# Performance work log

Hardware: AMD Instinct MI355X
Metric: run time of the kernel (lower is better)

The kernel has to match this reference:

```python
import jax, jax.numpy as jnp
import numpy as np

N, E, IN, H, L, NB, G = 50000, 300000, 64, 256, 4, 181, 64
EPS = 1e-5
NEG_SLOPE = 0.2


def segment_softmax(e, seg, n):
    m = jax.ops.segment_max(e, seg, num_segments=n)
    a = jnp.exp(e - m[seg])
    d = jax.ops.segment_sum(a, seg, num_segments=n)
    return a / d[seg]


def setup_inputs() -> dict:
    key = jax.random.key(0)
    ks = jax.random.split(key, 32)
    p = lambda k, shape, fan: (jax.random.normal(k, shape, jnp.float32) / np.sqrt(fan)).astype(jnp.float32)
    inp = {}
    inp["x"] = jax.random.normal(ks[0], (N, IN), jnp.float32)
    inp["edge_index"] = jax.random.randint(ks[1], (2, E), 0, N, jnp.int64)
    inp["batch"] = jnp.sort(jax.random.randint(ks[2], (N,), 0, G, jnp.int64))
    inp["W_in"] = p(ks[3], (H, IN), IN); inp["b_in"] = jnp.zeros((H,), jnp.float32)
    inp["Wl"] = p(ks[4], (L, H, H), H); inp["bl"] = jnp.zeros((L, H), jnp.float32)
    inp["Wr"] = p(ks[5], (L, H, H), H); inp["br"] = jnp.zeros((L, H), jnp.float32)
    inp["att"] = p(ks[6], (L, H), H)
    inp["bias_c"] = jnp.zeros((L, H), jnp.float32)
    inp["ln_g"] = jnp.ones((L, H), jnp.float32); inp["ln_b"] = jnp.zeros((L, H), jnp.float32)
    inp["Wg1"] = p(ks[7], (H, H), H); inp["bg1"] = jnp.zeros((H,), jnp.float32)
    inp["Wg2"] = p(ks[8], (1, H), H); inp["bg2"] = jnp.zeros((1,), jnp.float32)
    inp["Ws"] = p(ks[9], (H, H), H); inp["bs"] = jnp.zeros((H,), jnp.float32)
    inp["Wc"] = p(ks[10], (NB, H), H); inp["bc"] = jnp.zeros((NB,), jnp.float32)
    inp["Wr1"] = p(ks[11], (128, H), H); inp["br1"] = jnp.zeros((128,), jnp.float32)
    inp["Wr2"] = p(ks[12], (1, 128), 128); inp["br2"] = jnp.zeros((1,), jnp.float32)
    return inp


def reference(x, edge_index, batch, W_in, b_in, Wl, bl, Wr, br, att, bias_c, ln_g, ln_b,
              Wg1, bg1, Wg2, bg2, Ws, bs, Wc, bc, Wr1, br1, Wr2, br2):
    n = x.shape[0]
    x = x @ W_in.T + b_in  # input projection -> [N,H]
    loops = jnp.arange(n)
    src = jnp.concatenate([edge_index[0], loops])  # GATv2 add_self_loops=True
    dst = jnp.concatenate([edge_index[1], loops])
    for l in range(L):
        x_res = x
        xl = x @ Wl[l].T + bl[l]  # lin_l (source)
        xr = x @ Wr[l].T + br[l]  # lin_r (target)
        h = jax.nn.leaky_relu(xl[src] + xr[dst], NEG_SLOPE)  # [E+N, H]
        e = h @ att[l]                                       # [E+N]
        alpha = segment_softmax(e, dst, n)
        out = jax.ops.segment_sum(alpha[:, None] * xl[src], dst, num_segments=n) + bias_c[l]
        mu = out.mean(-1, keepdims=True)
        var = out.var(-1, keepdims=True)
        out = (out - mu) / jnp.sqrt(var + EPS) * ln_g[l] + ln_b[l]
        x = jax.nn.relu(out) + x_res  # dropout is identity at eval
    gate = jax.nn.relu(x @ Wg1.T + bg1) @ Wg2.T + bg2  # [N,1]
    a = segment_softmax(gate[:, 0], batch, G)
    pooled = jax.ops.segment_sum(a[:, None] * x, batch, num_segments=G)  # [G,H]
    z = jax.nn.relu(pooled @ Ws.T + bs)
    cls_logits = z @ Wc.T + bc                                   # [G,NB]
    residual = jnp.tanh(jax.nn.relu(z @ Wr1.T + br1) @ Wr2.T + br2)[:, 0]  # [G]
    return cls_logits, residual
```

## Files before the change

### kernel.cpp

```cpp
#include <hip/hip_runtime.h>
#include <math.h>

#define N_NODES 50000
#define N_EDGES 300000
#define IN_DIM 64
#define H 256
#define LAYERS 4
#define NB 181
#define NGRAPH 64
#define EE (N_EDGES + N_NODES)
#define NEG_SLOPE 0.2f
#define LN_EPS 1e-5f

typedef unsigned short u16;
typedef __attribute__((ext_vector_type(8))) _Float16 half8;
typedef __attribute__((ext_vector_type(4))) float floatx4;
typedef __attribute__((ext_vector_type(2))) _Float16 h2;

__device__ __forceinline__ u16 f2h(float f) {
  _Float16 h = (_Float16)f;
  return __builtin_bit_cast(u16, h);
}
__device__ __forceinline__ float h2f(u16 b) {
  return (float)__builtin_bit_cast(_Float16, b);
}
__device__ __forceinline__ h2 u2h2(unsigned int u) {
  return __builtin_bit_cast(h2, u);
}
__device__ __forceinline__ float fdot2f(h2 a, h2 b, float c) {
  typedef __attribute__((ext_vector_type(2))) __fp16 hb;
  return __builtin_amdgcn_fdot2(__builtin_bit_cast(hb, a),
                                __builtin_bit_cast(hb, b), c, false);
}

__device__ __forceinline__ float wave_reduce_sum(float v) {
  #pragma unroll
  for (int off = 32; off > 0; off >>= 1) v += __shfl_xor(v, off, 64);
  return v;
}

__device__ __forceinline__ float half_reduce_sum(float v) {
  v += __shfl_xor(v, 1, 64);
  v += __shfl_xor(v, 2, 64);
  v += __shfl_xor(v, 4, 64);
  v += __shfl_xor(v, 8, 64);
  v += __shfl_xor(v, 16, 64);
  return v;
}

__global__ void cast_weights_kernel(
    const float* __restrict__ Wg1,
    const float* __restrict__ Wl, const float* __restrict__ Wr,
    u16* __restrict__ wg1_h, u16* __restrict__ wl_h, u16* __restrict__ wr_h)
{
  int i = blockIdx.x * 256 + threadIdx.x;
  int which = blockIdx.y;
  const float* s; u16* dd; int n4;
  if (which == 0)      { s = Wg1;  dd = wg1_h; n4 = H * H / 4; }
  else if (which == 1) { s = Wl;   dd = wl_h;  n4 = LAYERS * H * H / 4; }
  else                 { s = Wr;   dd = wr_h;  n4 = LAYERS * H * H / 4; }
  if (i < n4) {
    float4 f = ((const float4*)s)[i];
    ushort4 o;
    o.x = f2h(f.x); o.y = f2h(f.y); o.z = f2h(f.z); o.w = f2h(f.w);
    ((ushort4*)dd)[i] = o;
  }
}

__global__ void init_kernel(int* __restrict__ cnt,
                            float* __restrict__ gate, const float* __restrict__ bg2,
                            const int* __restrict__ batch,
                            int* __restrict__ gstart, int* __restrict__ gend) {
  int i = blockIdx.x * 256 + threadIdx.x;
  if (i < N_NODES) {
    cnt[i] = 1;
    gate[i] = bg2[0];
    int b = batch[i];
    if (i == 0 || batch[i - 1] != b) gstart[b] = i;
    if (i == N_NODES - 1 || batch[i + 1] != b) gend[b] = i + 1;
  }
}

__global__ void count_edges_kernel(const int* __restrict__ dst, int* __restrict__ cnt) {
  int e = blockIdx.x * 256 + threadIdx.x;
  if (e < N_EDGES) atomicAdd(&cnt[dst[e]], 1);
}

__global__ void scan_blocks_kernel(const int* __restrict__ cnt, int* __restrict__ partial,
                                   int* __restrict__ bsums, int n) {
  __shared__ int buf[256];
  int tid = threadIdx.x;
  int i = blockIdx.x * 256 + tid;
  buf[tid] = (i < n) ? cnt[i] : 0;
  __syncthreads();
  #pragma unroll
  for (int off = 1; off < 256; off <<= 1) {
    int t = (tid >= off) ? buf[tid - off] : 0;
    __syncthreads();
    buf[tid] += t;
    __syncthreads();
  }
  if (i < n) partial[i] = buf[tid];
  if (tid == 255) bsums[blockIdx.x] = buf[255];
}

__global__ void scan_sums_kernel(int* __restrict__ bsums, int nblk) {
  __shared__ int buf[256];
  int tid = threadIdx.x;
  buf[tid] = (tid < nblk) ? bsums[tid] : 0;
  __syncthreads();
  #pragma unroll
  for (int off = 1; off < 256; off <<= 1) {
    int t = (tid >= off) ? buf[tid - off] : 0;
    __syncthreads();
    buf[tid] += t;
    __syncthreads();
  }
  if (tid < nblk) bsums[tid] = buf[tid];
}

__global__ void scan_write_kernel(const int* __restrict__ partial, const int* __restrict__ bsums,
                                  const int* __restrict__ cnt,
                                  int* __restrict__ rowp, int* __restrict__ col,
                                  int* __restrict__ fillpos, int n) {
  int i = blockIdx.x * 256 + threadIdx.x;
  if (i < n) {
    int b = blockIdx.x;
    int off = (b > 0) ? bsums[b - 1] : 0;
    int r1 = partial[i] + off;
    rowp[i + 1] = r1;
    if (i == 0) rowp[0] = 0;
    int p = r1 - cnt[i];
    col[p] = i;
    fillpos[i] = p + 1;
  }
}

__global__ void fill_edges_kernel(const int* __restrict__ src, const int* __restrict__ dst,
                                  int* __restrict__ fillpos, int* __restrict__ col) {
  int e = blockIdx.x * 256 + threadIdx.x;
  if (e < N_EDGES) {
    int d = dst[e];
    int p = atomicAdd(&fillpos[d], 1);
    col[p] = src[e];
  }
}

#define GTM 128
#define GTK 64
#define LDB 72
#define SSTR 132

__global__ __launch_bounds__(256) void gemm_proj_kernel(
    const float* __restrict__ A, const float* __restrict__ W,
    const float* __restrict__ bias, u16* __restrict__ outh, int M)
{
  __shared__ u16 smem[2 * GTM * LDB];
  u16* As = smem;
  u16* Bs = smem + GTM * LDB;
  int tid = threadIdx.x;
  int lane = tid & 63;
  int wave = tid >> 6;
  int wm = (wave >> 1) * 64;
  int wn = (wave & 1) * 64;
  int bm = blockIdx.y * GTM;
  int n0 = blockIdx.x * 128;

  floatx4 zero4 = {0.f, 0.f, 0.f, 0.f};
  floatx4 acc[4][4];
  #pragma unroll
  for (int i = 0; i < 4; i++)
    #pragma unroll
    for (int j = 0; j < 4; j++) acc[i][j] = zero4;

  int q8 = (lane >> 4) * 8;
  int mrow = lane & 15;

  {
    int r0 = tid >> 4;
    int c4 = (tid & 15) * 4;
    #pragma unroll
    for (int p = 0; p < 8; p++) {
      int row = r0 + p * 16;
      int gr = bm + row;
      float4 av = {0.f, 0.f, 0.f, 0.f};
      if (gr < M) av = *(const float4*)&A[(size_t)gr * IN_DIM + c4];
      ushort4 oa;
      oa.x = f2h(av.x); oa.y = f2h(av.y); oa.z = f2h(av.z); oa.w = f2h(av.w);
      *(ushort4*)&As[row * LDB + c4] = oa;
      float4 bv = *(const float4*)&W[(size_t)(n0 + row) * IN_DIM + c4];
      ushort4 ob;
      ob.x = f2h(bv.x); ob.y = f2h(bv.y); ob.z = f2h(bv.z); ob.w = f2h(bv.w);
      *(ushort4*)&Bs[row * LDB + c4] = ob;
    }
  }
  __syncthreads();
  #pragma unroll
  for (int h = 0; h < 2; h++) {
    half8 af[4], bf[4];
    #pragma unroll
    for (int i = 0; i < 4; i++)
      af[i] = *(const half8*)&As[(wm + i * 16 + mrow) * LDB + h * 32 + q8];
    #pragma unroll
    for (int j = 0; j < 4; j++)
      bf[j] = *(const half8*)&Bs[(wn + j * 16 + mrow) * LDB + h * 32 + q8];
    #pragma unroll
    for (int i = 0; i < 4; i++)
      #pragma unroll
      for (int j = 0; j < 4; j++)
        acc[i][j] = __builtin_amdgcn_mfma_f32_16x16x32_f16(af[i], bf[j], acc[i][j], 0, 0, 0);
  }

  __syncthreads();
  u16* stage = smem;
  int ccol = lane & 15;
  int crow4 = (lane >> 4) * 4;
  #pragma unroll
  for (int j = 0; j < 4; j++) {
    float bv = bias[n0 + wn + j * 16 + ccol];
    #pragma unroll
    for (int i = 0; i < 4; i++) {
      #pragma unroll
      for (int r = 0; r < 4; r++) {
        int row = wm + i * 16 + crow4 + r;
        stage[row * SSTR + wn + j * 16 + ccol] = f2h(acc[i][j][r] + bv);
      }
    }
  }
  __syncthreads();
  int rr = tid >> 1;
  int c0 = (tid & 1) * 64;
  int grow = bm + rr;
  if (grow < M) {
    const ushort4* sp = (const ushort4*)&stage[rr * SSTR + c0];
    ushort4* gp = (ushort4*)&outh[(size_t)grow * H + n0 + c0];
    #pragma unroll
    for (int q = 0; q < 16; q++) gp[q] = sp[q];
  }
}

#define DTM 64
#define SSTR2 132

__global__ __launch_bounds__(256) void gemm_dual3_kernel(
    const u16* __restrict__ A, const u16* __restrict__ Wlb, const u16* __restrict__ Wrb,
    const float* __restrict__ biasL, const float* __restrict__ biasR,
    u16* __restrict__ outL, u16* __restrict__ outR, int M)
{
  __shared__ u16 As[DTM * LDB];
  __shared__ u16 Bs[128 * LDB];
  int tid = threadIdx.x;
  int lane = tid & 63;
  int wave = tid >> 6;
  int wn = wave * 32;
  int nt = blockIdx.x;
  int bm = blockIdx.y * DTM;
  const u16* W = (nt < 2) ? Wlb : Wrb;
  const float* bias = (nt < 2) ? biasL : biasR;
  u16* outp = (nt < 2) ? outL : outR;
  int n0 = (nt & 1) * 128;
  int mrow = lane & 15;
  int q8 = (lane >> 4) * 8;
  int ccol = lane & 15;
  int crow4 = (lane >> 4) * 4;
  int lr = tid >> 3;
  int lc = (tid & 7) * 8;

  floatx4 zero4 = {0.f, 0.f, 0.f, 0.f};
  floatx4 acc[4][2];
  #pragma unroll
  for (int i = 0; i < 4; i++) {
    acc[i][0] = zero4;
    acc[i][1] = zero4;
  }

  for (int k0 = 0; k0 < H; k0 += 64) {
    __syncthreads();
    #pragma unroll
    for (int p = 0; p < 2; p++) {
      int row = lr + p * 32;
      int gr = bm + row;
      uint4 av = {0, 0, 0, 0};
      if (gr < M) av = *(const uint4*)&A[(size_t)gr * H + k0 + lc];
      *(uint4*)&As[row * LDB + lc] = av;
    }
    #pragma unroll
    for (int p = 0; p < 4; p++) {
      int row = lr + p * 32;
      uint4 bv = *(const uint4*)&W[(size_t)(n0 + row) * H + k0 + lc];
      *(uint4*)&Bs[row * LDB + lc] = bv;
    }
    __syncthreads();
    #pragma unroll
    for (int h = 0; h < 2; h++) {
      half8 af[4], bf[2];
      #pragma unroll
      for (int i = 0; i < 4; i++)
        af[i] = *(const half8*)&As[(i * 16 + mrow) * LDB + h * 32 + q8];
      #pragma unroll
      for (int j = 0; j < 2; j++)
        bf[j] = *(const half8*)&Bs[(wn + j * 16 + mrow) * LDB + h * 32 + q8];
      #pragma unroll
      for (int i = 0; i < 4; i++)
        #pragma unroll
        for (int j = 0; j < 2; j++)
          acc[i][j] = __builtin_amdgcn_mfma_f32_16x16x32_f16(af[i], bf[j], acc[i][j], 0, 0, 0);
    }
  }

  __syncthreads();
  u16* stage = Bs;
  #pragma unroll
  for (int j = 0; j < 2; j++) {
    float bv = bias[n0 + wn + j * 16 + ccol];
    #pragma unroll
    for (int i = 0; i < 4; i++) {
      #pragma unroll
      for (int r = 0; r < 4; r++) {
        int row = i * 16 + crow4 + r;
        stage[row * SSTR2 + wn + j * 16 + ccol] = f2h(acc[i][j][r] + bv);
      }
    }
  }
  __syncthreads();
  #pragma unroll
  for (int pass = 0; pass < 4; pass++) {
    int row = pass * 16 + (tid >> 4);
    int cu = (tid & 15) * 8;
    int grow = bm + row;
    if (grow < M) {
      *(uint4*)&outp[(size_t)grow * H + n0 + cu] =
          *(const uint4*)&stage[row * SSTR2 + cu];
    }
  }
}

__global__ __launch_bounds__(256) void gemm_gate2_kernel(
    const u16* __restrict__ A, const u16* __restrict__ W,
    const float* __restrict__ bias, const float* __restrict__ Wg2,
    float* __restrict__ gate, int M)
{
  __shared__ u16 As[DTM * LDB];
  __shared__ u16 Bs[128 * LDB];
  int tid = threadIdx.x;
  int lane = tid & 63;
  int wave = tid >> 6;
  int wn = wave * 32;
  int n0 = blockIdx.x * 128;
  int bm = blockIdx.y * DTM;
  int mrow = lane & 15;
  int q8 = (lane >> 4) * 8;
  int ccol = lane & 15;
  int crow4 = (lane >> 4) * 4;
  int lr = tid >> 3;
  int lc = (tid & 7) * 8;

  floatx4 zero4 = {0.f, 0.f, 0.f, 0.f};
  floatx4 acc[4][2];
  #pragma unroll
  for (int i = 0; i < 4; i++) {
    acc[i][0] = zero4;
    acc[i][1] = zero4;
  }

  for (int k0 = 0; k0 < H; k0 += 64) {
    __syncthreads();
    #pragma unroll
    for (int p = 0; p < 2; p++) {
      int row = lr + p * 32;
      int gr = bm + row;
      uint4 av = {0, 0, 0, 0};
      if (gr < M) av = *(const uint4*)&A[(size_t)gr * H + k0 + lc];
      *(uint4*)&As[row * LDB + lc] = av;
    }
    #pragma unroll
    for (int p = 0; p < 4; p++) {
      int row = lr + p * 32;
      uint4 bv = *(const uint4*)&W[(size_t)(n0 + row) * H + k0 + lc];
      *(uint4*)&Bs[row * LDB + lc] = bv;
    }
    __syncthreads();
    #pragma unroll
    for (int h = 0; h < 2; h++) {
      half8 af[4], bf[2];
      #pragma unroll
      for (int i = 0; i < 4; i++)
        af[i] = *(const half8*)&As[(i * 16 + mrow) * LDB + h * 32 + q8];
      #pragma unroll
      for (int j = 0; j < 2; j++)
        bf[j] = *(const half8*)&Bs[(wn + j * 16 + mrow) * LDB + h * 32 + q8];
      #pragma unroll
      for (int i = 0; i < 4; i++)
        #pragma unroll
        for (int j = 0; j < 2; j++)
          acc[i][j] = __builtin_amdgcn_mfma_f32_16x16x32_f16(af[i], bf[j], acc[i][j], 0, 0, 0);
    }
  }

  float bv[2], wv[2];
  #pragma unroll
  for (int j = 0; j < 2; j++) {
    int c = n0 + wn + j * 16 + ccol;
    bv[j] = bias[c];
    wv[j] = Wg2[c];
  }
  #pragma unroll
  for (int i = 0; i < 4; i++) {
    #pragma unroll
    for (int r = 0; r < 4; r++) {
      float p = fmaxf(acc[i][0][r] + bv[0], 0.f) * wv[0]
              + fmaxf(acc[i][1][r] + bv[1], 0.f) * wv[1];
      p += __shfl_xor(p, 1, 64);
      p += __shfl_xor(p, 2, 64);
      p += __shfl_xor(p, 4, 64);
      p += __shfl_xor(p, 8, 64);
      int row = bm + i * 16 + crow4 + r;
      if ((lane & 15) == 0 && row < M) atomicAdd(&gate[row], p);
    }
  }
}

__global__ __launch_bounds__(256) void layer_fused_kernel(
    const u16* __restrict__ xl, const u16* __restrict__ xr,
    u16* __restrict__ xst,
    const int* __restrict__ rowp, const int* __restrict__ col,
    const float* __restrict__ att, const float* __restrict__ bias_c,
    const float* __restrict__ ln_g, const float* __restrict__ ln_b)
{
  int lane = threadIdx.x & 63;
  int v = blockIdx.x * 4 + (threadIdx.x >> 6);
  if (v >= N_NODES) return;
  int half = lane >> 5;
  int f8 = (lane & 31) << 3;

  float4 attA = *(const float4*)&att[f8];
  float4 attB = *(const float4*)&att[f8 + 4];
  h2 att0, att1, att2, att3;
  att0[0] = (_Float16)attA.x; att0[1] = (_Float16)attA.y;
  att1[0] = (_Float16)attA.z; att1[1] = (_Float16)attA.w;
  att2[0] = (_Float16)attB.x; att2[1] = (_Float16)attB.y;
  att3[0] = (_Float16)attB.z; att3[1] = (_Float16)attB.w;
  h2 nsl; nsl[0] = (_Float16)NEG_SLOPE; nsl[1] = (_Float16)NEG_SLOPE;

  size_t rowbase = (size_t)v * H + f8;
  uint4 xru = *(const uint4*)&xr[rowbase];
  h2 xr0 = u2h2(xru.x), xr1 = u2h2(xru.y), xr2 = u2h2(xru.z), xr3 = u2h2(xru.w);
  int beg = rowp[v], end = rowp[v + 1];

  uint4 su = *(const uint4*)&xl[rowbase];
  h2 s0 = u2h2(su.x), s1 = u2h2(su.y), s2 = u2h2(su.z), s3 = u2h2(su.w);
  float m;
  {
    h2 t; float pe = 0.f;
    t = s0 + xr0; t = __builtin_elementwise_max(t, t * nsl); pe = fdot2f(t, att0, pe);
    t = s1 + xr1; t = __builtin_elementwise_max(t, t * nsl); pe = fdot2f(t, att1, pe);
    t = s2 + xr2; t = __builtin_elementwise_max(t, t * nsl); pe = fdot2f(t, att2, pe);
    t = s3 + xr3; t = __builtin_elementwise_max(t, t * nsl); pe = fdot2f(t, att3, pe);
    m = half_reduce_sum(pe);
  }
  float wself = half ? 0.f : 1.f;
  float d = wself;
  float o0 = wself * (float)s0[0], o1 = wself * (float)s0[1];
  float o2 = wself * (float)s1[0], o3 = wself * (float)s1[1];
  float o4 = wself * (float)s2[0], o5 = wself * (float)s2[1];
  float o6 = wself * (float)s3[0], o7 = wself * (float)s3[1];

  int p = beg + 1;
  for (; p + 4 <= end; p += 4) {
    int ua = col[p + half];
    int ub = col[p + 2 + half];
    uint4 A = *(const uint4*)&xl[(size_t)ua * H + f8];
    uint4 B = *(const uint4*)&xl[(size_t)ub * H + f8];
    h2 a0 = u2h2(A.x), a1 = u2h2(A.y), a2 = u2h2(A.z), a3 = u2h2(A.w);
    h2 b0 = u2h2(B.x), b1 = u2h2(B.y), b2 = u2h2(B.z), b3 = u2h2(B.w);
    float pa = 0.f, pb = 0.f;
    {
      h2 t;
      t = a0 + xr0; t = __builtin_elementwise_max(t, t * nsl); pa = fdot2f(t, att0, pa);
      t = b0 + xr0; t = __builtin_elementwise_max(t, t * nsl); pb = fdot2f(t, att0, pb);
      t = a1 + xr1; t = __builtin_elementwise_max(t, t * nsl); pa = fdot2f(t, att1, pa);
      t = b1 + xr1; t = __builtin_elementwise_max(t, t * nsl); pb = fdot2f(t, att1, pb);
      t = a2 + xr2; t = __builtin_elementwise_max(t, t * nsl); pa = fdot2f(t, att2, pa);
      t = b2 + xr2; t = __builtin_elementwise_max(t, t * nsl); pb = fdot2f(t, att2, pb);
      t = a3 + xr3; t = __builtin_elementwise_max(t, t * nsl); pa = fdot2f(t, att3, pa);
      t = b3 + xr3; t = __builtin_elementwise_max(t, t * nsl); pb = fdot2f(t, att3, pb);
    }
    #pragma unroll
    for (int off = 1; off <= 16; off <<= 1) {
      pa += __shfl_xor(pa, off, 64);
      pb += __shfl_xor(pb, off, 64);
    }
    float wa = __expf(pa - m);
    float wb = __expf(pb - m);
    d += wa + wb;
    o0 = fmaf(wa, (float)a0[0], fmaf(wb, (float)b0[0], o0));
    o1 = fmaf(wa, (float)a0[1], fmaf(wb, (float)b0[1], o1));
    o2 = fmaf(wa, (float)a1[0], fmaf(wb, (float)b1[0], o2));
    o3 = fmaf(wa, (float)a1[1], fmaf(wb, (float)b1[1], o3));
    o4 = fmaf(wa, (float)a2[0], fmaf(wb, (float)b2[0], o4));
    o5 = fmaf(wa, (float)a2[1], fmaf(wb, (float)b2[1], o5));
    o6 = fmaf(wa, (float)a3[0], fmaf(wb, (float)b3[0], o6));
    o7 = fmaf(wa, (float)a3[1], fmaf(wb, (float)b3[1], o7));
  }
  for (; p + 2 <= end; p += 2) {
    int ua = col[p + half];
    uint4 A = *(const uint4*)&xl[(size_t)ua * H + f8];
    h2 a0 = u2h2(A.x), a1 = u2h2(A.y), a2 = u2h2(A.z), a3 = u2h2(A.w);
    float pa = 0.f;
    {
      h2 t;
      t = a0 + xr0; t = __builtin_elementwise_max(t, t * nsl); pa = fdot2f(t, att0, pa);
      t = a1 + xr1; t = __builtin_elementwise_max(t, t * nsl); pa = fdot2f(t, att1, pa);
      t = a2 + xr2; t = __builtin_elementwise_max(t, t * nsl); pa = fdot2f(t, att2, pa);
      t = a3 + xr3; t = __builtin_elementwise_max(t, t * nsl); pa = fdot2f(t, att3, pa);
    }
    pa = half_reduce_sum(pa);
    float wa = __expf(pa - m);
    d += wa;
    o0 = fmaf(wa, (float)a0[0], o0);
    o1 = fmaf(wa, (float)a0[1], o1);
    o2 = fmaf(wa, (float)a1[0], o2);
    o3 = fmaf(wa, (float)a1[1], o3);
    o4 = fmaf(wa, (float)a2[0], o4);
    o5 = fmaf(wa, (float)a2[1], o5);
    o6 = fmaf(wa, (float)a3[0], o6);
    o7 = fmaf(wa, (float)a3[1], o7);
  }
  if (p < end) {
    int ua = col[p];
    uint4 A = *(const uint4*)&xl[(size_t)ua * H + f8];
    h2 a0 = u2h2(A.x), a1 = u2h2(A.y), a2 = u2h2(A.z), a3 = u2h2(A.w);
    float pa = 0.f;
    {
      h2 t;
      t = a0 + xr0; t = __builtin_elementwise_max(t, t * nsl); pa = fdot2f(t, att0, pa);
      t = a1 + xr1; t = __builtin_elementwise_max(t, t * nsl); pa = fdot2f(t, att1, pa);
      t = a2 + xr2; t = __builtin_elementwise_max(t, t * nsl); pa = fdot2f(t, att2, pa);
      t = a3 + xr3; t = __builtin_elementwise_max(t, t * nsl); pa = fdot2f(t, att3, pa);
    }
    pa = half_reduce_sum(pa);
    float wa = __expf(pa - m) * wself;
    d += wa;
    o0 = fmaf(wa, (float)a0[0], o0);
    o1 = fmaf(wa, (float)a0[1], o1);
    o2 = fmaf(wa, (float)a1[0], o2);
    o3 = fmaf(wa, (float)a1[1], o3);
    o4 = fmaf(wa, (float)a2[0], o4);
    o5 = fmaf(wa, (float)a2[1], o5);
    o6 = fmaf(wa, (float)a3[0], o6);
    o7 = fmaf(wa, (float)a3[1], o7);
  }

  d += __shfl_xor(d, 32, 64);
  o0 += __shfl_xor(o0, 32, 64);
  o1 += __shfl_xor(o1, 32, 64);
  o2 += __shfl_xor(o2, 32, 64);
  o3 += __shfl_xor(o3, 32, 64);
  o4 += __shfl_xor(o4, 32, 64);
  o5 += __shfl_xor(o5, 32, 64);
  o6 += __shfl_xor(o6, 32, 64);
  o7 += __shfl_xor(o7, 32, 64);

  float invd = 1.0f / d;
  float4 bcA = *(const float4*)&bias_c[f8];
  float4 bcB = *(const float4*)&bias_c[f8 + 4];
  o0 = o0 * invd + bcA.x; o1 = o1 * invd + bcA.y;
  o2 = o2 * invd + bcA.z; o3 = o3 * invd + bcA.w;
  o4 = o4 * invd + bcB.x; o5 = o5 * invd + bcB.y;
  o6 = o6 * invd + bcB.z; o7 = o7 * invd + bcB.w;

  float s = ((o0 + o1) + (o2 + o3)) + ((o4 + o5) + (o6 + o7));
  s = wave_reduce_sum(s);
  float mean = s * (1.0f / (2 * H));
  float c0 = o0 - mean, c1 = o1 - mean, c2 = o2 - mean, c3 = o3 - mean;
  float c4 = o4 - mean, c5 = o5 - mean, c6 = o6 - mean, c7 = o7 - mean;
  float sq = ((c0 * c0 + c1 * c1) + (c2 * c2 + c3 * c3))
           + ((c4 * c4 + c5 * c5) + (c6 * c6 + c7 * c7));
  sq = wave_reduce_sum(sq);
  float rstd = rsqrtf(sq * (1.0f / (2 * H)) + LN_EPS);

  float4 gA = *(const float4*)&ln_g[f8];
  float4 gB = *(const float4*)&ln_g[f8 + 4];
  float4 bA = *(const float4*)&ln_b[f8];
  float4 bB = *(const float4*)&ln_b[f8 + 4];
  uint4 xres = *(const uint4*)&xst[rowbase];
  h2 r0 = u2h2(xres.x), r1 = u2h2(xres.y), r2 = u2h2(xres.z), r3 = u2h2(xres.w);
  float y0 = fmaxf(fmaf(c0 * rstd, gA.x, bA.x), 0.f) + (float)r0[0];
  float y1 = fmaxf(fmaf(c1 * rstd, gA.y, bA.y), 0.f) + (float)r0[1];
  float y2 = fmaxf(fmaf(c2 * rstd, gA.z, bA.z), 0.f) + (float)r1[0];
  float y3 = fmaxf(fmaf(c3 * rstd, gA.w, bA.w), 0.f) + (float)r1[1];
  float y4 = fmaxf(fmaf(c4 * rstd, gB.x, bB.x), 0.f) + (float)r2[0];
  float y5 = fmaxf(fmaf(c5 * rstd, gB.y, bB.y), 0.f) + (float)r2[1];
  float y6 = fmaxf(fmaf(c6 * rstd, gB.z, bB.z), 0.f) + (float)r3[0];
  float y7 = fmaxf(fmaf(c7 * rstd, gB.w, bB.w), 0.f) + (float)r3[1];
  if (!half) {
    uint4 outv;
    outv.x = (unsigned)f2h(y0) | ((unsigned)f2h(y1) << 16);
    outv.y = (unsigned)f2h(y2) | ((unsigned)f2h(y3) << 16);
    outv.z = (unsigned)f2h(y4) | ((unsigned)f2h(y5) << 16);
    outv.w = (unsigned)f2h(y6) | ((unsigned)f2h(y7) << 16);
    *(uint4*)&xst[rowbase] = outv;
  }
}

__global__ __launch_bounds__(256) void pool_prep_kernel(
    const float* __restrict__ gate, const int* __restrict__ gstart,
    const int* __restrict__ gend, float* __restrict__ gmax, float* __restrict__ gdinv,
    float* __restrict__ pooled)
{
  __shared__ float red[256];
  int g = blockIdx.x, tid = threadIdx.x;
  pooled[(size_t)g * H + tid] = 0.f;
  int s = gstart[g], e = gend[g];
  float lm = -INFINITY;
  for (int i = s + tid; i < e; i += 256) lm = fmaxf(lm, gate[i]);
  red[tid] = lm;
  __syncthreads();
  for (int off = 128; off; off >>= 1) {
    if (tid < off) red[tid] = fmaxf(red[tid], red[tid + off]);
    __syncthreads();
  }
  float m = red[0];
  __syncthreads();
  float lsum = 0.0f;
  for (int i = s + tid; i < e; i += 256) lsum += __expf(gate[i] - m);
  red[tid] = lsum;
  __syncthreads();
  for (int off = 128; off; off >>= 1) {
    if (tid < off) red[tid] += red[tid + off];
    __syncthreads();
  }
  if (tid == 0) {
    gmax[g] = m;
    gdinv[g] = (s < e) ? 1.0f / red[0] : 0.0f;
  }
}

__global__ __launch_bounds__(256) void pool_accum_kernel(
    const float* __restrict__ gate, const u16* __restrict__ xh,
    const int* __restrict__ batch, const float* __restrict__ gmax,
    const float* __restrict__ gdinv, float* __restrict__ pooled)
{
  __shared__ float wl[64];
  __shared__ int gl[64];
  int b0 = blockIdx.x * 64;
  int tid = threadIdx.x;
  if (tid < 64) {
    int v = b0 + tid;
    if (v < N_NODES) {
      int g = batch[v];
      gl[tid] = g;
      wl[tid] = __expf(gate[v] - gmax[g]) * gdinv[g];
    } else {
      gl[tid] = -1;
      wl[tid] = 0.f;
    }
  }
  __syncthreads();
  int cnt = min(64, N_NODES - b0);
  float acc = 0.f;
  int cur = gl[0];
  for (int j = 0; j < cnt; j++) {
    int g = gl[j];
    if (g != cur) {
      atomicAdd(&pooled[(size_t)cur * H + tid], acc);
      acc = 0.f;
      cur = g;
    }
    acc += wl[j] * h2f(xh[(size_t)(b0 + j) * H + tid]);
  }
  if (cur >= 0) atomicAdd(&pooled[(size_t)cur * H + tid], acc);
}

__global__ __launch_bounds__(256) void head_kernel(
    const float* __restrict__ pooled,
    const float* __restrict__ Ws, const float* __restrict__ bs,
    const float* __restrict__ Wc, const float* __restrict__ bc,
    const float* __restrict__ Wr1, const float* __restrict__ br1,
    const float* __restrict__ Wr2, const float* __restrict__ br2,
    float* __restrict__ out)
{
  __shared__ float psh[256];
  __shared__ float zsh[256];
  __shared__ float r1sh[128];
  int g = blockIdx.x, tid = threadIdx.x;
  psh[tid] = pooled[(size_t)g * H + tid];
  __syncthreads();
  {
    float acc = bs[tid];
    const float4* wr = (const float4*)&Ws[(size_t)tid * H];
    for (int k4 = 0; k4 < H / 4; k4++) {
      float4 wv = wr[k4];
      float4 av = *(const float4*)&psh[k4 * 4];
      acc += av.x * wv.x + av.y * wv.y + av.z * wv.z + av.w * wv.w;
    }
    zsh[tid] = fmaxf(acc, 0.f);
  }
  __syncthreads();
  if (tid < NB) {
    float acc = bc[tid];
    const float4* wr = (const float4*)&Wc[(size_t)tid * H];
    for (int k4 = 0; k4 < H / 4; k4++) {
      float4 wv = wr[k4];
      float4 av = *(const float4*)&zsh[k4 * 4];
      acc += av.x * wv.x + av.y * wv.y + av.z * wv.z + av.w * wv.w;
    }
    out[(size_t)g * NB + tid] = acc;
  }
  if (tid < 128) {
    float acc = br1[tid];
    const float4* wr = (const float4*)&Wr1[(size_t)tid * H];
    for (int k4 = 0; k4 < H / 4; k4++) {
      float4 wv = wr[k4];
      float4 av = *(const float4*)&zsh[k4 * 4];
      acc += av.x * wv.x + av.y * wv.y + av.z * wv.z + av.w * wv.w;
    }
    r1sh[tid] = fmaxf(acc, 0.f);
  }
  __syncthreads();
  if (tid < 64) {
    float s2 = r1sh[tid] * Wr2[tid] + r1sh[tid + 64] * Wr2[tid + 64];
    s2 = wave_reduce_sum(s2);
    if (tid == 0) out[(size_t)NGRAPH * NB + g] = tanhf(s2 + br2[0]);
  }
}

extern "C" void kernel_launch(void* const* d_in, const int* in_sizes, int n_in,
                              void* d_out, int out_size, void* d_ws, size_t ws_size,
                              hipStream_t stream) {
  const float* x_in   = (const float*)d_in[0];
  const int*   eidx   = (const int*)d_in[1];
  const int*   batch  = (const int*)d_in[2];
  const float* W_in   = (const float*)d_in[3];
  const float* b_in   = (const float*)d_in[4];
  const float* Wl     = (const float*)d_in[5];
  const float* bl     = (const float*)d_in[6];
  const float* Wr     = (const float*)d_in[7];
  const float* br     = (const float*)d_in[8];
  const float* att    = (const float*)d_in[9];
  const float* bias_c = (const float*)d_in[10];
  const float* ln_g   = (const float*)d_in[11];
  const float* ln_b   = (const float*)d_in[12];
  const float* Wg1    = (const float*)d_in[13];
  const float* bg1    = (const float*)d_in[14];
  const float* Wg2    = (const float*)d_in[15];
  const float* bg2    = (const float*)d_in[16];
  const float* Ws     = (const float*)d_in[17];
  const float* bs     = (const float*)d_in[18];
  const float* Wc     = (const float*)d_in[19];
  const float* bc     = (const float*)d_in[20];
  const float* Wr1    = (const float*)d_in[21];
  const float* br1    = (const float*)d_in[22];
  const float* Wr2    = (const float*)d_in[23];
  const float* br2    = (const float*)d_in[24];
  float* out = (float*)d_out;

  char* w = (char*)d_ws;
  u16* x_h    = (u16*)w;    w += sizeof(u16) * (size_t)N_NODES * H;
  u16* xl_h   = (u16*)w;    w += sizeof(u16) * (size_t)N_NODES * H;
  u16* xr_h   = (u16*)w;    w += sizeof(u16) * (size_t)N_NODES * H;
  u16* wl_h   = (u16*)w;    w += sizeof(u16) * (size_t)LAYERS * H * H;
  u16* wr_h   = (u16*)w;    w += sizeof(u16) * (size_t)LAYERS * H * H;
  u16* wg1_h  = (u16*)w;    w += sizeof(u16) * (size_t)H * H;
  float* pooled = (float*)w; w += sizeof(float) * NGRAPH * H;
  float* gate = (float*)w;  w += sizeof(float) * N_NODES;
  float* gmax = (float*)w;  w += sizeof(float) * NGRAPH;
  float* gdinv= (float*)w;  w += sizeof(float) * NGRAPH;
  int* cnt    = (int*)w;    w += sizeof(int) * N_NODES;
  int* rowp   = (int*)w;    w += sizeof(int) * (N_NODES + 1);
  int* col    = (int*)w;    w += sizeof(int) * EE;
  int* partial= (int*)w;    w += sizeof(int) * N_NODES;
  int* bsums  = (int*)w;    w += sizeof(int) * 256;
  int* gstart = (int*)w;    w += sizeof(int) * NGRAPH;
  int* gend   = (int*)w;    w += sizeof(int) * NGRAPH;
  (void)ws_size; (void)n_in; (void)in_sizes; (void)out_size;

  const int* src = eidx;
  const int* dst = eidx + N_EDGES;
  int nblkN = (N_NODES + 255) / 256;
  int nblkE = (N_EDGES + 255) / 256;
  int mtiles = (N_NODES + GTM - 1) / GTM;
  int mtiles2 = (N_NODES + DTM - 1) / DTM;

  init_kernel<<<nblkN, 256, 0, stream>>>(cnt, gate, bg2, batch, gstart, gend);
  count_edges_kernel<<<nblkE, 256, 0, stream>>>(dst, cnt);
  scan_blocks_kernel<<<nblkN, 256, 0, stream>>>(cnt, partial, bsums, N_NODES);
  scan_sums_kernel<<<1, 256, 0, stream>>>(bsums, nblkN);
  scan_write_kernel<<<nblkN, 256, 0, stream>>>(partial, bsums, cnt, rowp, col, cnt, N_NODES);
  fill_edges_kernel<<<nblkE, 256, 0, stream>>>(src, dst, cnt, col);

  {
    int maxn4 = LAYERS * H * H / 4;
    dim3 gcast((maxn4 + 255) / 256, 3);
    cast_weights_kernel<<<gcast, 256, 0, stream>>>(Wg1, Wl, Wr, wg1_h, wl_h, wr_h);
  }

  dim3 gproj(2, mtiles);
  gemm_proj_kernel<<<gproj, 256, 0, stream>>>(x_in, W_in, b_in, x_h, N_NODES);

  int nblkV = N_NODES / 4;
  dim3 gdual(4, mtiles2);
  for (int l = 0; l < LAYERS; l++) {
    gemm_dual3_kernel<<<gdual, 256, 0, stream>>>(x_h,
        wl_h + (size_t)l * H * H, wr_h + (size_t)l * H * H,
        bl + l * H, br + l * H, xl_h, xr_h, N_NODES);
    layer_fused_kernel<<<nblkV, 256, 0, stream>>>(xl_h, xr_h, x_h, rowp, col,
        att + l * H, bias_c + l * H, ln_g + l * H, ln_b + l * H);
  }

  dim3 ggate(2, mtiles2);
  gemm_gate2_kernel<<<ggate, 256, 0, stream>>>(x_h, wg1_h, bg1, Wg2, gate, N_NODES);

  pool_prep_kernel<<<NGRAPH, 256, 0, stream>>>(gate, gstart, gend, gmax, gdinv, pooled);
  pool_accum_kernel<<<(N_NODES + 63) / 64, 256, 0, stream>>>(gate, x_h, batch, gmax, gdinv, pooled);

  head_kernel<<<NGRAPH, 256, 0, stream>>>(pooled, Ws, bs, Wc, bc, Wr1, br1, Wr2, br2, out);
}
```

Before: 559.7 us.

## Map one graph node per half-wave in fused GATv2 layer kernel

The fused attention/aggregation/LayerNorm kernel now gives each 32-lane half-wave its own destination node, instead of splitting one node's edges across both halves of a 64-lane wave. The loop runs for the larger of the two halves' iteration counts and masks out invalid edges, so the separate remainder loops and the cross-half reductions of the accumulators go away. LayerNorm statistics use half-wave reductions, all lanes write output, and the residual load is issued early alongside the other row loads. Half as many waves are launched. The risk is idle lanes when the two nodes sharing a wave have unequal degrees, plus somewhat higher register pressure from the hoisted loads.

```diff
diff --git a/kernel.cpp b/kernel.cpp
--- a/kernel.cpp
+++ b/kernel.cpp
@@ -428,9 +428,9 @@
     const float* __restrict__ ln_g, const float* __restrict__ ln_b)
 {
   int lane = threadIdx.x & 63;
-  int v = blockIdx.x * 4 + (threadIdx.x >> 6);
-  if (v >= N_NODES) return;
+  int wid = blockIdx.x * 4 + (threadIdx.x >> 6);
   int half = lane >> 5;
+  int v = wid * 2 + half;
   int f8 = (lane & 31) << 3;
 
   float4 attA = *(const float4*)&att[f8];
@@ -443,12 +443,14 @@
   h2 nsl; nsl[0] = (_Float16)NEG_SLOPE; nsl[1] = (_Float16)NEG_SLOPE;
 
   size_t rowbase = (size_t)v * H + f8;
+  int beg = rowp[v], end = rowp[v + 1];
   uint4 xru = *(const uint4*)&xr[rowbase];
+  uint4 su  = *(const uint4*)&xl[rowbase];
+  uint4 xres = *(const uint4*)&xst[rowbase];
+
   h2 xr0 = u2h2(xru.x), xr1 = u2h2(xru.y), xr2 = u2h2(xru.z), xr3 = u2h2(xru.w);
-  int beg = rowp[v], end = rowp[v + 1];
-
-  uint4 su = *(const uint4*)&xl[rowbase];
   h2 s0 = u2h2(su.x), s1 = u2h2(su.y), s2 = u2h2(su.z), s3 = u2h2(su.w);
+
   float m;
   {
     h2 t; float pe = 0.f;
@@ -458,17 +460,23 @@
     t = s3 + xr3; t = __builtin_elementwise_max(t, t * nsl); pe = fdot2f(t, att3, pe);
     m = half_reduce_sum(pe);
   }
-  float wself = half ? 0.f : 1.f;
-  float d = wself;
-  float o0 = wself * (float)s0[0], o1 = wself * (float)s0[1];
-  float o2 = wself * (float)s1[0], o3 = wself * (float)s1[1];
-  float o4 = wself * (float)s2[0], o5 = wself * (float)s2[1];
-  float o6 = wself * (float)s3[0], o7 = wself * (float)s3[1];
+  float d = 1.0f;
+  float o0 = (float)s0[0], o1 = (float)s0[1];
+  float o2 = (float)s1[0], o3 = (float)s1[1];
+  float o4 = (float)s2[0], o5 = (float)s2[1];
+  float o6 = (float)s3[0], o7 = (float)s3[1];
 
   int p = beg + 1;
-  for (; p + 4 <= end; p += 4) {
-    int ua = col[p + half];
-    int ub = col[p + 2 + half];
+  int rem = end - p;
+  int it_half = (rem + 1) >> 1;
+  int it_other = __shfl_xor(it_half, 32, 64);
+  int iters = it_half > it_other ? it_half : it_other;
+
+  for (int i = 0; i < iters; i++) {
+    bool e0 = p < end;
+    bool e1 = p + 1 < end;
+    int ua = col[e0 ? p : beg];
+    int ub = col[e1 ? p + 1 : beg];
     uint4 A = *(const uint4*)&xl[(size_t)ua * H + f8];
     uint4 B = *(const uint4*)&xl[(size_t)ub * H + f8];
     h2 a0 = u2h2(A.x), a1 = u2h2(A.y), a2 = u2h2(A.z), a3 = u2h2(A.w);
@@ -490,8 +498,8 @@
       pa += __shfl_xor(pa, off, 64);
       pb += __shfl_xor(pb, off, 64);
     }
-    float wa = __expf(pa - m);
-    float wb = __expf(pb - m);
+    float wa = e0 ? __expf(pa - m) : 0.f;
+    float wb = e1 ? __expf(pb - m) : 0.f;
     d += wa + wb;
     o0 = fmaf(wa, (float)a0[0], fmaf(wb, (float)b0[0], o0));
     o1 = fmaf(wa, (float)a0[1], fmaf(wb, (float)b0[1], o1));
@@ -501,65 +509,8 @@
     o5 = fmaf(wa, (float)a2[1], fmaf(wb, (float)b2[1], o5));
     o6 = fmaf(wa, (float)a3[0], fmaf(wb, (float)b3[0], o6));
     o7 = fmaf(wa, (float)a3[1], fmaf(wb, (float)b3[1], o7));
-  }
-  for (; p + 2 <= end; p += 2) {
-    int ua = col[p + half];
-    uint4 A = *(const uint4*)&xl[(size_t)ua * H + f8];
-    h2 a0 = u2h2(A.x), a1 = u2h2(A.y), a2 = u2h2(A.z), a3 = u2h2(A.w);
-    float pa = 0.f;
-    {
-      h2 t;
-      t = a0 + xr0; t = __builtin_elementwise_max(t, t * nsl); pa = fdot2f(t, att0, pa);
-      t = a1 + xr1; t = __builtin_elementwise_max(t, t * nsl); pa = fdot2f(t, att1, pa);
-      t = a2 + xr2; t = __builtin_elementwise_max(t, t * nsl); pa = fdot2f(t, att2, pa);
-      t = a3 + xr3; t = __builtin_elementwise_max(t, t * nsl); pa = fdot2f(t, att3, pa);
-    }
-    pa = half_reduce_sum(pa);
-    float wa = __expf(pa - m);
-    d += wa;
-    o0 = fmaf(wa, (float)a0[0], o0);
-    o1 = fmaf(wa, (float)a0[1], o1);
-    o2 = fmaf(wa, (float)a1[0], o2);
-    o3 = fmaf(wa, (float)a1[1], o3);
-    o4 = fmaf(wa, (float)a2[0], o4);
-    o5 = fmaf(wa, (float)a2[1], o5);
-    o6 = fmaf(wa, (float)a3[0], o6);
-    o7 = fmaf(wa, (float)a3[1], o7);
-  }
-  if (p < end) {
-    int ua = col[p];
-    uint4 A = *(const uint4*)&xl[(size_t)ua * H + f8];
-    h2 a0 = u2h2(A.x), a1 = u2h2(A.y), a2 = u2h2(A.z), a3 = u2h2(A.w);
-    float pa = 0.f;
-    {
-      h2 t;
-      t = a0 + xr0; t = __builtin_elementwise_max(t, t * nsl); pa = fdot2f(t, att0, pa);
-      t = a1 + xr1; t = __builtin_elementwise_max(t, t * nsl); pa = fdot2f(t, att1, pa);
-      t = a2 + xr2; t = __builtin_elementwise_max(t, t * nsl); pa = fdot2f(t, att2, pa);
-      t = a3 + xr3; t = __builtin_elementwise_max(t, t * nsl); pa = fdot2f(t, att3, pa);
-    }
-    pa = half_reduce_sum(pa);
-    float wa = __expf(pa - m) * wself;
-    d += wa;
-    o0 = fmaf(wa, (float)a0[0], o0);
-    o1 = fmaf(wa, (float)a0[1], o1);
-    o2 = fmaf(wa, (float)a1[0], o2);
-    o3 = fmaf(wa, (float)a1[1], o3);
-    o4 = fmaf(wa, (float)a2[0], o4);
-    o5 = fmaf(wa, (float)a2[1], o5);
-    o6 = fmaf(wa, (float)a3[0], o6);
-    o7 = fmaf(wa, (float)a3[1], o7);
-  }
-
-  d += __shfl_xor(d, 32, 64);
-  o0 += __shfl_xor(o0, 32, 64);
-  o1 += __shfl_xor(o1, 32, 64);
-  o2 += __shfl_xor(o2, 32, 64);
-  o3 += __shfl_xor(o3, 32, 64);
-  o4 += __shfl_xor(o4, 32, 64);
-  o5 += __shfl_xor(o5, 32, 64);
-  o6 += __shfl_xor(o6, 32, 64);
-  o7 += __shfl_xor(o7, 32, 64);
+    p += 2;
+  }
 
   float invd = 1.0f / d;
   float4 bcA = *(const float4*)&bias_c[f8];
@@ -570,20 +521,19 @@
   o6 = o6 * invd + bcB.z; o7 = o7 * invd + bcB.w;
 
   float s = ((o0 + o1) + (o2 + o3)) + ((o4 + o5) + (o6 + o7));
-  s = wave_reduce_sum(s);
-  float mean = s * (1.0f / (2 * H));
+  s = half_reduce_sum(s);
+  float mean = s * (1.0f / H);
   float c0 = o0 - mean, c1 = o1 - mean, c2 = o2 - mean, c3 = o3 - mean;
   float c4 = o4 - mean, c5 = o5 - mean, c6 = o6 - mean, c7 = o7 - mean;
   float sq = ((c0 * c0 + c1 * c1) + (c2 * c2 + c3 * c3))
            + ((c4 * c4 + c5 * c5) + (c6 * c6 + c7 * c7));
-  sq = wave_reduce_sum(sq);
-  float rstd = rsqrtf(sq * (1.0f / (2 * H)) + LN_EPS);
+  sq = half_reduce_sum(sq);
+  float rstd = rsqrtf(sq * (1.0f / H) + LN_EPS);
 
   float4 gA = *(const float4*)&ln_g[f8];
   float4 gB = *(const float4*)&ln_g[f8 + 4];
   float4 bA = *(const float4*)&ln_b[f8];
   float4 bB = *(const float4*)&ln_b[f8 + 4];
-  uint4 xres = *(const uint4*)&xst[rowbase];
   h2 r0 = u2h2(xres.x), r1 = u2h2(xres.y), r2 = u2h2(xres.z), r3 = u2h2(xres.w);
   float y0 = fmaxf(fmaf(c0 * rstd, gA.x, bA.x), 0.f) + (float)r0[0];
   float y1 = fmaxf(fmaf(c1 * rstd, gA.y, bA.y), 0.f) + (float)r0[1];
@@ -593,14 +543,12 @@
   float y5 = fmaxf(fmaf(c5 * rstd, gB.y, bB.y), 0.f) + (float)r2[1];
   float y6 = fmaxf(fmaf(c6 * rstd, gB.z, bB.z), 0.f) + (float)r3[0];
   float y7 = fmaxf(fmaf(c7 * rstd, gB.w, bB.w), 0.f) + (float)r3[1];
-  if (!half) {
-    uint4 outv;
-    outv.x = (unsigned)f2h(y0) | ((unsigned)f2h(y1) << 16);
-    outv.y = (unsigned)f2h(y2) | ((unsigned)f2h(y3) << 16);
-    outv.z = (unsigned)f2h(y4) | ((unsigned)f2h(y5) << 16);
-    outv.w = (unsigned)f2h(y6) | ((unsigned)f2h(y7) << 16);
-    *(uint4*)&xst[rowbase] = outv;
-  }
+  uint4 outv;
+  outv.x = (unsigned)f2h(y0) | ((unsigned)f2h(y1) << 16);
+  outv.y = (unsigned)f2h(y2) | ((unsigned)f2h(y3) << 16);
+  outv.z = (unsigned)f2h(y4) | ((unsigned)f2h(y5) << 16);
+  outv.w = (unsigned)f2h(y6) | ((unsigned)f2h(y7) << 16);
+  *(uint4*)&xst[rowbase] = outv;
 }
 
 __global__ __launch_bounds__(256) void pool_prep_kernel(
@@ -798,7 +746,7 @@
   dim3 gproj(2, mtiles);
   gemm_proj_kernel<<<gproj, 256, 0, stream>>>(x_in, W_in, b_in, x_h, N_NODES);
 
-  int nblkV = N_NODES / 4;
+  int nblkV = (N_NODES / 2 + 3) / 4;
   dim3 gdual(4, mtiles2);
   for (int l = 0; l < LAYERS; l++) {
     gemm_dual3_kernel<<<gdual, 256, 0, stream>>>(x_h,
```

New measurement: 551.2 us. No clear change (-1.5%).
